# Kernel optimization log

Measured on AMD Instinct MI355X. Metric: run time of the kernel, lower is better.

Reference implementation:

```python
import jax, jax.numpy as jnp
import numpy as np

D_MODEL = 1024
NUM_HEADS = 16
D_K = D_MODEL // NUM_HEADS
SCALE = float(np.sqrt(D_K))


def setup_inputs() -> dict:
    key = jax.random.key(0)
    ks = jax.random.split(key, 11)
    B, S = 2, 2048
    s = 0.02
    return {
        "query": jax.random.normal(ks[0], (B, S, D_MODEL), dtype=jnp.float32),
        "key_in": jax.random.normal(ks[1], (B, S, D_MODEL), dtype=jnp.float32),
        "value": jax.random.normal(ks[2], (B, S, D_MODEL), dtype=jnp.float32),
        "w_q": jax.random.normal(ks[3], (D_MODEL, D_MODEL), dtype=jnp.float32) * s,
        "b_q": jnp.zeros((D_MODEL,), dtype=jnp.float32),
        "w_k": jax.random.normal(ks[4], (D_MODEL, D_MODEL), dtype=jnp.float32) * s,
        "b_k": jnp.zeros((D_MODEL,), dtype=jnp.float32),
        "w_v": jax.random.normal(ks[5], (D_MODEL, D_MODEL), dtype=jnp.float32) * s,
        "b_v": jnp.zeros((D_MODEL,), dtype=jnp.float32),
        "w_o": jax.random.normal(ks[6], (D_MODEL, D_MODEL), dtype=jnp.float32) * s,
        "b_o": jnp.zeros((D_MODEL,), dtype=jnp.float32),
    }


def _mha(query, key_in, value, w_q, b_q, w_k, b_k, w_v, b_v, w_o, b_o):
    B, S, _ = query.shape
    # linear projections (x @ W + b), split into heads: [B, H, S, Dk]
    def proj(x, w, b):
        y = x @ w + b
        return y.reshape(B, -1, NUM_HEADS, D_K).transpose(0, 2, 1, 3)

    Q = proj(query, w_q, b_q)
    K = proj(key_in, w_k, b_k)
    V = proj(value, w_v, b_v)

    # scores: [B, H, Sq, Sk]
    scores = jnp.einsum("bhqd,bhkd->bhqk", Q, K) / SCALE
    attn = jax.nn.softmax(scores, axis=-1)  # dropout is identity in eval mode
    out = jnp.einsum("bhqk,bhkd->bhqd", attn, V)
    out = out.transpose(0, 2, 1, 3).reshape(B, S, D_MODEL)
    return out @ w_o + b_o


def reference(query, key_in, value, w_q, b_q, w_k, b_k, w_v, b_v, w_o, b_o):
    return _mha(query, key_in, value, w_q, b_q, w_k, b_k, w_v, b_v, w_o, b_o)
```

## Files before the change

### kernel.cpp

```cpp
#include <hip/hip_runtime.h>
#include <cstdint>

#define S_LEN 2048
#define DMODEL 1024
#define NHEADS 16
#define DK 64
#define BATCH 2
#define M_TOT 4096

typedef __attribute__((ext_vector_type(8))) short  short8;
typedef __attribute__((ext_vector_type(4))) float  f32x4;

__device__ __forceinline__ ushort f2bf(float f) {
    union { float f; uint32_t u; } v; v.f = f;
    uint32_t r = (v.u + 0x7fffu + ((v.u >> 16) & 1u)) >> 16;
    return (ushort)r;
}
__device__ __forceinline__ float bf2f(ushort u) {
    union { uint32_t u; float f; } v; v.u = ((uint32_t)u) << 16;
    return v.f;
}

__device__ __forceinline__ void gl_lds16(const void* g, void* l) {
    __builtin_amdgcn_global_load_lds(
        (const __attribute__((address_space(1))) void*)(g),
        (__attribute__((address_space(3))) void*)(l), 16, 0, 0);
}

__global__ __launch_bounds__(256)
void conv3_kernel(const float* __restrict__ a0, const float* __restrict__ a1,
                  const float* __restrict__ a2, ushort* __restrict__ o0,
                  ushort* __restrict__ o1, ushort* __restrict__ o2, int n8)
{
    const float*  in  = blockIdx.z == 0 ? a0 : (blockIdx.z == 1 ? a1 : a2);
    ushort*       out = blockIdx.z == 0 ? o0 : (blockIdx.z == 1 ? o1 : o2);
    int i = blockIdx.x * 256 + threadIdx.x;
    const int stride = gridDim.x * 256;
    for (; i < n8; i += stride) {
        const float4* p = (const float4*)(in + (size_t)i * 8);
        float4 a = p[0], b = p[1];
        ushort r[8];
        r[0]=f2bf(a.x); r[1]=f2bf(a.y); r[2]=f2bf(a.z); r[3]=f2bf(a.w);
        r[4]=f2bf(b.x); r[5]=f2bf(b.y); r[6]=f2bf(b.z); r[7]=f2bf(b.w);
        *(ushort4*)(out + (size_t)i * 8)     = *(ushort4*)&r[0];
        *(ushort4*)(out + (size_t)i * 8 + 4) = *(ushort4*)&r[4];
    }
}

__global__ __launch_bounds__(256)
void wtrans3_kernel(const float* __restrict__ wq, const float* __restrict__ wk,
                    const float* __restrict__ wv, ushort* __restrict__ oq,
                    ushort* __restrict__ ok, ushort* __restrict__ ov)
{
    const float* w  = blockIdx.z == 0 ? wq : (blockIdx.z == 1 ? wk : wv);
    ushort*      hi = blockIdx.z == 0 ? oq : (blockIdx.z == 1 ? ok : ov);

    __shared__ float t[64][65];
    const int n0 = blockIdx.x * 64, k0 = blockIdx.y * 64;
    const int r  = threadIdx.x >> 2;
    const int cb = (threadIdx.x & 3) * 16;

    #pragma unroll
    for (int j = 0; j < 4; ++j) {
        float4 v = *(const float4*)(w + (size_t)(k0 + r) * DMODEL + n0 + cb + j * 4);
        t[r][cb + j*4 + 0] = v.x;
        t[r][cb + j*4 + 1] = v.y;
        t[r][cb + j*4 + 2] = v.z;
        t[r][cb + j*4 + 3] = v.w;
    }
    __syncthreads();

    ushort h8[16];
    #pragma unroll
    for (int j = 0; j < 16; ++j) h8[j] = f2bf(t[cb + j][r]);
    ushort* dsth = hi + (size_t)(n0 + r) * DMODEL + k0 + cb;
    *(ushort4*)(dsth + 0)  = *(ushort4*)&h8[0];
    *(ushort4*)(dsth + 4)  = *(ushort4*)&h8[4];
    *(ushort4*)(dsth + 8)  = *(ushort4*)&h8[8];
    *(ushort4*)(dsth + 12) = *(ushort4*)&h8[12];
}

__global__ __launch_bounds__(256)
void wtrans_o_kernel(const float* __restrict__ w, ushort* __restrict__ hi,
                     ushort* __restrict__ lo)
{
    __shared__ float t[64][65];
    const int n0 = blockIdx.x * 64, k0 = blockIdx.y * 64;
    const int r  = threadIdx.x >> 2;
    const int cb = (threadIdx.x & 3) * 16;

    #pragma unroll
    for (int j = 0; j < 4; ++j) {
        float4 v = *(const float4*)(w + (size_t)(k0 + r) * DMODEL + n0 + cb + j * 4);
        t[r][cb + j*4 + 0] = v.x;
        t[r][cb + j*4 + 1] = v.y;
        t[r][cb + j*4 + 2] = v.z;
        t[r][cb + j*4 + 3] = v.w;
    }
    __syncthreads();

    ushort h8[16], l8[16];
    #pragma unroll
    for (int j = 0; j < 16; ++j) {
        float x = t[cb + j][r];
        ushort h = f2bf(x);
        h8[j] = h;
        l8[j] = f2bf(x - bf2f(h));
    }
    ushort* dsth = hi + (size_t)(n0 + r) * DMODEL + k0 + cb;
    ushort* dstl = lo + (size_t)(n0 + r) * DMODEL + k0 + cb;
    #pragma unroll
    for (int j = 0; j < 4; ++j) {
        *(ushort4*)(dsth + j*4) = *(ushort4*)&h8[j*4];
        *(ushort4*)(dstl + j*4) = *(ushort4*)&l8[j*4];
    }
}

template<int OMODE>
__global__ __launch_bounds__(256)
void gemm_bf16_kernel(const ushort* __restrict__ A, const ushort* __restrict__ Bt,
                      const float* __restrict__ bias, ushort* __restrict__ out,
                      float oscale)
{
    __shared__ __align__(16) ushort lds[2][12288];

    const int t = threadIdx.x, wv = t >> 6, lane = t & 63;
    const int c = lane & 15, g = lane >> 4;
    const int m0 = blockIdx.y * 128, n0 = blockIdx.x * 64;
    const int wr = wv >> 1, wc = wv & 1;
    const int lrow = lane >> 3, lcol = lane & 7;

    f32x4 acc[4][2];
    #pragma unroll
    for (int i = 0; i < 4; ++i)
        #pragma unroll
        for (int j = 0; j < 2; ++j)
            acc[i][j] = (f32x4){0.f, 0.f, 0.f, 0.f};

    auto stage = [&](int buf, int kt) {
        #pragma unroll
        for (int j = 0; j < 6; ++j) {
            const int ci = wv * 6 + j;
            ushort* dst = &lds[buf][ci * 512];
            const ushort* src;
            if (ci < 16) {
                const int row  = ci * 8 + lrow;
                const int colb = (lcol * 16) ^ ((row & 7) << 4);
                src = A + (size_t)(m0 + row) * 1024 + kt * 64 + (colb >> 1);
            } else {
                const int row  = (ci - 16) * 8 + lrow;
                const int colb = (lcol * 16) ^ ((row & 7) << 4);
                src = Bt + (size_t)(n0 + row) * 1024 + kt * 64 + (colb >> 1);
            }
            gl_lds16(src, dst);
        }
    };

    stage(0, 0);
    __syncthreads();

    for (int kt = 0; kt < 16; ++kt) {
        const int cur = kt & 1;
        if (kt < 15) stage(cur ^ 1, kt + 1);

        const char* la = (const char*)&lds[cur][0];
        const char* lb = (const char*)&lds[cur][8192];
        #pragma unroll
        for (int kk = 0; kk < 2; ++kk) {
            short8 af[4], bf[2];
            #pragma unroll
            for (int mf = 0; mf < 4; ++mf) {
                const int row = wr * 64 + mf * 16 + c;
                af[mf] = *(const short8*)(la + row * 128 +
                          ((kk * 64 + g * 16) ^ ((c & 7) << 4)));
            }
            #pragma unroll
            for (int nf = 0; nf < 2; ++nf) {
                const int row = wc * 32 + nf * 16 + c;
                bf[nf] = *(const short8*)(lb + row * 128 +
                          ((kk * 64 + g * 16) ^ ((c & 7) << 4)));
            }
            #pragma unroll
            for (int mf = 0; mf < 4; ++mf)
                #pragma unroll
                for (int nf = 0; nf < 2; ++nf)
                    acc[mf][nf] = __builtin_amdgcn_mfma_f32_16x16x32_bf16(
                        af[mf], bf[nf], acc[mf][nf], 0, 0, 0);
        }
        __syncthreads();
    }

    const int b      = m0 >> 11;
    const int s_base = m0 & 2047;
    #pragma unroll
    for (int nf = 0; nf < 2; ++nf) {
        const int ncol = n0 + wc * 32 + nf * 16 + c;
        const float bv = bias[ncol];
        const int h = ncol >> 6, dk = ncol & 63;
        #pragma unroll
        for (int mf = 0; mf < 4; ++mf) {
            if (OMODE == 1) {
                #pragma unroll
                for (int j = 0; j < 4; ++j) {
                    const int s = s_base + wr * 64 + mf * 16 + g * 4 + j;
                    out[(((size_t)(b * NHEADS + h) * S_LEN + s) * DK) + dk] =
                        f2bf((acc[mf][nf][j] + bv) * oscale);
                }
            } else {
                ushort4 v4;
                v4.x = f2bf((acc[mf][nf][0] + bv) * oscale);
                v4.y = f2bf((acc[mf][nf][1] + bv) * oscale);
                v4.z = f2bf((acc[mf][nf][2] + bv) * oscale);
                v4.w = f2bf((acc[mf][nf][3] + bv) * oscale);
                const int s = s_base + wr * 64 + mf * 16 + g * 4;
                *(ushort4*)&out[((size_t)(b * NHEADS + h) * DK + dk) * S_LEN + s] = v4;
            }
        }
    }
}

__global__ __launch_bounds__(256)
void gemm_split_kernel(const ushort* __restrict__ Ahi, const ushort* __restrict__ Alo,
                       const ushort* __restrict__ Bhi, const ushort* __restrict__ Blo,
                       const float* __restrict__ bias, float* __restrict__ out)
{
    __shared__ __align__(16) ushort lds[24576];

    const int t = threadIdx.x, wv = t >> 6, lane = t & 63;
    const int c = lane & 15, g = lane >> 4;
    const int m0 = blockIdx.y * 128, n0 = blockIdx.x * 64;
    const int wr = wv >> 1, wc = wv & 1;
    const int lrow = lane >> 3, lcol = lane & 7;

    f32x4 acc[4][2];
    #pragma unroll
    for (int i = 0; i < 4; ++i)
        #pragma unroll
        for (int j = 0; j < 2; ++j)
            acc[i][j] = (f32x4){0.f, 0.f, 0.f, 0.f};

    for (int kt = 0; kt < 16; ++kt) {
        if (kt) __syncthreads();
        #pragma unroll
        for (int j = 0; j < 12; ++j) {
            const int ci = wv * 12 + j;
            ushort* dst = &lds[ci * 512];
            const ushort* src;
            int row, colb;
            if (ci < 16) {
                row = ci * 8 + lrow; colb = (lcol*16) ^ ((row&7)<<4);
                src = Ahi + (size_t)(m0+row)*1024 + kt*64 + (colb>>1);
            } else if (ci < 32) {
                row = (ci-16)*8 + lrow; colb = (lcol*16) ^ ((row&7)<<4);
                src = Alo + (size_t)(m0+row)*1024 + kt*64 + (colb>>1);
            } else if (ci < 40) {
                row = (ci-32)*8 + lrow; colb = (lcol*16) ^ ((row&7)<<4);
                src = Bhi + (size_t)(n0+row)*1024 + kt*64 + (colb>>1);
            } else {
                row = (ci-40)*8 + lrow; colb = (lcol*16) ^ ((row&7)<<4);
                src = Blo + (size_t)(n0+row)*1024 + kt*64 + (colb>>1);
            }
            gl_lds16(src, dst);
        }
        __syncthreads();

        const char* lah = (const char*)&lds[0];
        const char* lal = (const char*)&lds[8192];
        const char* lbh = (const char*)&lds[16384];
        const char* lbl = (const char*)&lds[20480];
        #pragma unroll
        for (int kk = 0; kk < 2; ++kk) {
            short8 ah[4], al[4], bh[2], bl[2];
            #pragma unroll
            for (int mf = 0; mf < 4; ++mf) {
                const int row = wr*64 + mf*16 + c;
                const int off = row*128 + ((kk*64 + g*16) ^ ((c&7)<<4));
                ah[mf] = *(const short8*)(lah + off);
                al[mf] = *(const short8*)(lal + off);
            }
            #pragma unroll
            for (int nf = 0; nf < 2; ++nf) {
                const int row = wc*32 + nf*16 + c;
                const int off = row*128 + ((kk*64 + g*16) ^ ((c&7)<<4));
                bh[nf] = *(const short8*)(lbh + off);
                bl[nf] = *(const short8*)(lbl + off);
            }
            #pragma unroll
            for (int mf = 0; mf < 4; ++mf)
                #pragma unroll
                for (int nf = 0; nf < 2; ++nf) {
                    acc[mf][nf] = __builtin_amdgcn_mfma_f32_16x16x32_bf16(ah[mf], bh[nf], acc[mf][nf], 0,0,0);
                    acc[mf][nf] = __builtin_amdgcn_mfma_f32_16x16x32_bf16(ah[mf], bl[nf], acc[mf][nf], 0,0,0);
                    acc[mf][nf] = __builtin_amdgcn_mfma_f32_16x16x32_bf16(al[mf], bh[nf], acc[mf][nf], 0,0,0);
                }
        }
    }

    #pragma unroll
    for (int nf = 0; nf < 2; ++nf) {
        const int ncol = n0 + wc*32 + nf*16 + c;
        const float bv = bias[ncol];
        #pragma unroll
        for (int mf = 0; mf < 4; ++mf)
            #pragma unroll
            for (int j = 0; j < 4; ++j) {
                const int m = m0 + wr*64 + mf*16 + g*4 + j;
                out[(size_t)m * 1024 + ncol] = acc[mf][nf][j] + bv;
            }
    }
}

__global__ __launch_bounds__(256, 4)
void attn_kernel3(const ushort* __restrict__ Qh, const ushort* __restrict__ Kh,
                  const ushort* __restrict__ Vt, ushort* __restrict__ ctx_hi,
                  ushort* __restrict__ ctx_lo)
{
    __shared__ __align__(16) ushort   KV[2][8192];
    __shared__ __align__(16) uint32_t Plds[4][512];

    const int t = threadIdx.x, wv = t >> 6, lane = t & 63;
    const int c = lane & 15, g = lane >> 4;
    const int bh = blockIdx.y;
    const int q0 = blockIdx.x * 64 + wv * 16;
    const int lrow = lane >> 3, lcol = lane & 7;

    const ushort* Kb = Kh + (size_t)bh * S_LEN * DK;
    const ushort* Vb = Vt + (size_t)bh * DK * S_LEN;

    const ushort* Qb = Qh + ((size_t)bh * S_LEN + q0 + c) * DK;
    short8 qf[2];
    qf[0] = *(const short8*)(Qb + g * 8);
    qf[1] = *(const short8*)(Qb + 32 + g * 8);

    auto stage = [&](int buf, int k0) {
        #pragma unroll
        for (int j = 0; j < 4; ++j) {
            const int ci = wv * 4 + j;
            ushort* dst = &KV[buf][ci * 512];
            const ushort* src;
            if (ci < 8) {
                const int row  = ci * 8 + lrow;
                const int colb = (lcol * 16) ^ ((row & 7) << 4);
                src = Kb + (size_t)(k0 + row) * DK + (colb >> 1);
            } else {
                const int row  = (ci - 8) * 8 + lrow;
                const int colb = (lcol * 16) ^ ((row & 7) << 4);
                src = Vb + (size_t)row * S_LEN + k0 + (colb >> 1);
            }
            gl_lds16(src, dst);
        }
    };

    float m = -3.0e38f, l = 0.f;
    f32x4 acc_o[4];
    #pragma unroll
    for (int i = 0; i < 4; ++i) acc_o[i] = (f32x4){0.f, 0.f, 0.f, 0.f};

    char* Pb = (char*)&Plds[wv][0];
    const int a7 = (c & 7) << 4;

    stage(0, 0);
    __syncthreads();

    for (int kt = 0; kt < 32; ++kt) {
        const int cur = kt & 1;
        if (kt < 31) stage(cur ^ 1, (kt + 1) * 64);

        const char* Kl = (const char*)&KV[cur][0];
        const char* Vl = (const char*)&KV[cur][4096];

        f32x4 sa[4];
        #pragma unroll
        for (int kb = 0; kb < 4; ++kb) sa[kb] = (f32x4){0.f,0.f,0.f,0.f};
        #pragma unroll
        for (int kb = 0; kb < 4; ++kb) {
            const int row = kb * 16 + c;
            #pragma unroll
            for (int h = 0; h < 2; ++h) {
                short8 kf = *(const short8*)(Kl + row * 128 + ((h * 64 + g * 16) ^ a7));
                sa[kb] = __builtin_amdgcn_mfma_f32_16x16x32_bf16(kf, qf[h], sa[kb], 0,0,0);
            }
        }

        float mt = sa[0][0];
        #pragma unroll
        for (int kb = 0; kb < 4; ++kb)
            #pragma unroll
            for (int j = 0; j < 4; ++j) mt = fmaxf(mt, sa[kb][j]);
        mt = fmaxf(mt, __shfl_xor(mt, 16));
        mt = fmaxf(mt, __shfl_xor(mt, 32));

        if (__any(mt > m + 8.f)) {
            const float mnew = fmaxf(m, mt);
            const float corr = __builtin_amdgcn_exp2f(m - mnew);
            float corrj[4];
            #pragma unroll
            for (int j = 0; j < 4; ++j)
                corrj[j] = __shfl(corr, (lane & 48) | (g * 4 + j));
            #pragma unroll
            for (int db = 0; db < 4; ++db)
                #pragma unroll
                for (int j = 0; j < 4; ++j) acc_o[db][j] *= corrj[j];
            l *= corr;
            m = mnew;
        }

        float p[16], ps = 0.f;
        #pragma unroll
        for (int kb = 0; kb < 4; ++kb)
            #pragma unroll
            for (int j = 0; j < 4; ++j) {
                float pp = __builtin_amdgcn_exp2f(sa[kb][j] - m);
                p[kb * 4 + j] = pp;
                ps += pp;
            }
        ps += __shfl_xor(ps, 16);
        ps += __shfl_xor(ps, 32);
        l += ps;

        uint32_t u[8];
        #pragma unroll
        for (int i = 0; i < 8; ++i)
            asm("v_cvt_pk_bf16_f32 %0, %1, %2"
                : "=v"(u[i]) : "v"(p[2*i]), "v"(p[2*i+1]));
        #pragma unroll
        for (int kb = 0; kb < 4; ++kb) {
            uint2 w2; w2.x = u[2*kb]; w2.y = u[2*kb+1];
            *(uint2*)(Pb + c * 128 + ((kb * 32 + g * 8) ^ a7)) = w2;
        }
        short8 pa0 = *(const short8*)(Pb + c * 128 + ((g * 16) ^ a7));
        short8 pa1 = *(const short8*)(Pb + c * 128 + ((64 + g * 16) ^ a7));

        #pragma unroll
        for (int db = 0; db < 4; ++db) {
            const int row = db * 16 + c;
            short8 vf0 = *(const short8*)(Vl + row * 128 + ((g * 16) ^ a7));
            short8 vf1 = *(const short8*)(Vl + row * 128 + ((64 + g * 16) ^ a7));
            acc_o[db] = __builtin_amdgcn_mfma_f32_16x16x32_bf16(pa0, vf0, acc_o[db], 0,0,0);
            acc_o[db] = __builtin_amdgcn_mfma_f32_16x16x32_bf16(pa1, vf1, acc_o[db], 0,0,0);
        }
        __syncthreads();
    }

    float invj[4];
    #pragma unroll
    for (int j = 0; j < 4; ++j)
        invj[j] = 1.f / __shfl(l, (lane & 48) | (g * 4 + j));

    const int b = bh >> 4, h = bh & 15;
    #pragma unroll
    for (int db = 0; db < 4; ++db)
        #pragma unroll
        for (int j = 0; j < 4; ++j) {
            const float val = acc_o[db][j] * invj[j];
            const ushort hi = f2bf(val);
            const ushort lo = f2bf(val - bf2f(hi));
            const size_t idx = ((size_t)b * S_LEN + q0 + g * 4 + j) * DMODEL
                             + h * DK + db * 16 + c;
            ctx_hi[idx] = hi;
            ctx_lo[idx] = lo;
        }
}

extern "C" void kernel_launch(void* const* d_in, const int* in_sizes, int n_in,
                              void* d_out, int out_size, void* d_ws, size_t ws_size,
                              hipStream_t stream)
{
    const float* query  = (const float*)d_in[0];
    const float* key_in = (const float*)d_in[1];
    const float* value  = (const float*)d_in[2];
    const float* w_q = (const float*)d_in[3];
    const float* b_q = (const float*)d_in[4];
    const float* w_k = (const float*)d_in[5];
    const float* b_k = (const float*)d_in[6];
    const float* w_v = (const float*)d_in[7];
    const float* b_v = (const float*)d_in[8];
    const float* w_o = (const float*)d_in[9];
    const float* b_o = (const float*)d_in[10];
    float* out = (float*)d_out;

    const size_t E4M = (size_t)M_TOT * DMODEL;
    const size_t E1M = (size_t)DMODEL * DMODEL;

    ushort* ws = (ushort*)d_ws;
    ushort* Aq    = ws;
    ushort* Ak    = Aq + E4M;
    ushort* Av    = Ak + E4M;
    ushort* Qh    = Av + E4M;
    ushort* Kh    = Qh + E4M;
    ushort* Vt    = Kh + E4M;
    ushort* Wq    = Vt + E4M;
    ushort* Wk    = Wq + E1M;
    ushort* Wv    = Wk + E1M;
    ushort* Wo_hi = Wv + E1M;
    ushort* Wo_lo = Wo_hi + E1M;
    ushort* ctx_hi = Aq;
    ushort* ctx_lo = Ak;

    const float qscale = 0.125f * 1.44269504088896340736f;

    dim3 blk(256);
    hipLaunchKernelGGL(conv3_kernel, dim3(512, 1, 3), blk, 0, stream,
                       query, key_in, value, Aq, Ak, Av, (int)(E4M / 8));
    hipLaunchKernelGGL(wtrans3_kernel, dim3(16, 16, 3), blk, 0, stream,
                       w_q, w_k, w_v, Wq, Wk, Wv);
    hipLaunchKernelGGL(wtrans_o_kernel, dim3(16, 16), blk, 0, stream,
                       w_o, Wo_hi, Wo_lo);

    dim3 ggrd(DMODEL / 64, M_TOT / 128);
    hipLaunchKernelGGL((gemm_bf16_kernel<1>), ggrd, blk, 0, stream, Aq, Wq, b_q, Qh, qscale);
    hipLaunchKernelGGL((gemm_bf16_kernel<1>), ggrd, blk, 0, stream, Ak, Wk, b_k, Kh, 1.0f);
    hipLaunchKernelGGL((gemm_bf16_kernel<2>), ggrd, blk, 0, stream, Av, Wv, b_v, Vt, 1.0f);

    dim3 agrd(S_LEN / 64, BATCH * NHEADS);
    hipLaunchKernelGGL(attn_kernel3, agrd, blk, 0, stream, Qh, Kh, Vt, ctx_hi, ctx_lo);

    hipLaunchKernelGGL(gemm_split_kernel, ggrd, blk, 0, stream,
                       ctx_hi, ctx_lo, Wo_hi, Wo_lo, b_o, out);
}
```

Before: 160.1 us.

## Rewrite attention with 32x32 MFMA tiles and register-only P exchange

The attention kernel moves from 16x16x32 to 32x32x16 bf16 MFMA, with each wave owning 32 query rows and each block 128 queries. The P matrix is handed from the score MFMA layout to the PV operand layout with v_permlane32_swap in registers instead of a round trip through LDS, which removes the per-wave P buffer. Staging addresses are precomputed once outside the loop. The cost is more registers per wave (launch bounds drop to 2 blocks) and half as many blocks, which lowers occupancy and parallelism.

```diff
diff --git a/kernel.cpp b/kernel.cpp
--- a/kernel.cpp
+++ b/kernel.cpp
@@ -8,8 +8,9 @@
 #define BATCH 2
 #define M_TOT 4096
 
-typedef __attribute__((ext_vector_type(8))) short  short8;
-typedef __attribute__((ext_vector_type(4))) float  f32x4;
+typedef __attribute__((ext_vector_type(8)))  short  short8;
+typedef __attribute__((ext_vector_type(4)))  float  f32x4;
+typedef __attribute__((ext_vector_type(16))) float  f32x16;
 
 __device__ __forceinline__ ushort f2bf(float f) {
     union { float f; uint32_t u; } v; v.f = f;
@@ -310,54 +311,64 @@
     }
 }
 
-__global__ __launch_bounds__(256, 4)
-void attn_kernel3(const ushort* __restrict__ Qh, const ushort* __restrict__ Kh,
+__global__ __launch_bounds__(256, 2)
+void attn_kernel4(const ushort* __restrict__ Qh, const ushort* __restrict__ Kh,
                   const ushort* __restrict__ Vt, ushort* __restrict__ ctx_hi,
                   ushort* __restrict__ ctx_lo)
 {
-    __shared__ __align__(16) ushort   KV[2][8192];
-    __shared__ __align__(16) uint32_t Plds[4][512];
-
-    const int t = threadIdx.x, wv = t >> 6, lane = t & 63;
-    const int c = lane & 15, g = lane >> 4;
+    __shared__ __align__(16) ushort KV[2][8192];
+
+    const int t  = threadIdx.x, wv = t >> 6, lane = t & 63;
+    const int q  = lane & 31;
+    const int hi = lane >> 5;
     const int bh = blockIdx.y;
-    const int q0 = blockIdx.x * 64 + wv * 16;
-    const int lrow = lane >> 3, lcol = lane & 7;
+    const int q0 = blockIdx.x * 128 + wv * 32;
 
     const ushort* Kb = Kh + (size_t)bh * S_LEN * DK;
     const ushort* Vb = Vt + (size_t)bh * DK * S_LEN;
-
-    const ushort* Qb = Qh + ((size_t)bh * S_LEN + q0 + c) * DK;
-    short8 qf[2];
-    qf[0] = *(const short8*)(Qb + g * 8);
-    qf[1] = *(const short8*)(Qb + 32 + g * 8);
-
+    const ushort* Qb = Qh + ((size_t)bh * S_LEN + q0 + q) * DK;
+
+    short8 qf[4];
+    #pragma unroll
+    for (int s = 0; s < 4; ++s)
+        qf[s] = *(const short8*)(Qb + s * 16 + hi * 8);
+
+    const ushort* sbase[4];
+    int sstr[4];
+    char* dbase[4];
+    #pragma unroll
+    for (int j = 0; j < 4; ++j) {
+        const int D = (j * 256 + t) * 16;
+        dbase[j] = (char*)&KV[0][0] + D;
+        if (D < 8192) {
+            const int row = D >> 7;
+            const int X   = D & 127;
+            const int Xs  = X ^ ((row & 7) << 4);
+            sbase[j] = Kb + row * DK + (Xs >> 1);
+            sstr[j]  = DK;
+        } else {
+            const int Y   = D - 8192;
+            const int kk  = Y >> 12;
+            const int Z   = Y & 4095;
+            const int r   = Z >> 7;
+            const int gsl = ((Z & 127) >> 4) ^ (r & 7);
+            const int d   = r + ((gsl >> 2) << 5);
+            sbase[j] = Vb + (size_t)d * S_LEN + kk * 32 + (gsl & 3) * 8;
+            sstr[j]  = 1;
+        }
+    }
     auto stage = [&](int buf, int k0) {
         #pragma unroll
-        for (int j = 0; j < 4; ++j) {
-            const int ci = wv * 4 + j;
-            ushort* dst = &KV[buf][ci * 512];
-            const ushort* src;
-            if (ci < 8) {
-                const int row  = ci * 8 + lrow;
-                const int colb = (lcol * 16) ^ ((row & 7) << 4);
-                src = Kb + (size_t)(k0 + row) * DK + (colb >> 1);
-            } else {
-                const int row  = (ci - 8) * 8 + lrow;
-                const int colb = (lcol * 16) ^ ((row & 7) << 4);
-                src = Vb + (size_t)row * S_LEN + k0 + (colb >> 1);
-            }
-            gl_lds16(src, dst);
-        }
+        for (int j = 0; j < 4; ++j)
+            gl_lds16(sbase[j] + (size_t)k0 * sstr[j], dbase[j] + buf * 16384);
     };
 
     float m = -3.0e38f, l = 0.f;
-    f32x4 acc_o[4];
-    #pragma unroll
-    for (int i = 0; i < 4; ++i) acc_o[i] = (f32x4){0.f, 0.f, 0.f, 0.f};
-
-    char* Pb = (char*)&Plds[wv][0];
-    const int a7 = (c & 7) << 4;
+    f32x16 accO[2];
+    #pragma unroll
+    for (int i = 0; i < 16; ++i) { accO[0][i] = 0.f; accO[1][i] = 0.f; }
+
+    const int swz = (q & 7) << 4;
 
     stage(0, 0);
     __syncthreads();
@@ -367,98 +378,81 @@
         if (kt < 31) stage(cur ^ 1, (kt + 1) * 64);
 
         const char* Kl = (const char*)&KV[cur][0];
-        const char* Vl = (const char*)&KV[cur][4096];
-
-        f32x4 sa[4];
-        #pragma unroll
-        for (int kb = 0; kb < 4; ++kb) sa[kb] = (f32x4){0.f,0.f,0.f,0.f};
-        #pragma unroll
-        for (int kb = 0; kb < 4; ++kb) {
-            const int row = kb * 16 + c;
-            #pragma unroll
-            for (int h = 0; h < 2; ++h) {
-                short8 kf = *(const short8*)(Kl + row * 128 + ((h * 64 + g * 16) ^ a7));
-                sa[kb] = __builtin_amdgcn_mfma_f32_16x16x32_bf16(kf, qf[h], sa[kb], 0,0,0);
-            }
-        }
-
-        float mt = sa[0][0];
-        #pragma unroll
-        for (int kb = 0; kb < 4; ++kb)
-            #pragma unroll
-            for (int j = 0; j < 4; ++j) mt = fmaxf(mt, sa[kb][j]);
-        mt = fmaxf(mt, __shfl_xor(mt, 16));
-        mt = fmaxf(mt, __shfl_xor(mt, 32));
-
-        if (__any(mt > m + 8.f)) {
-            const float mnew = fmaxf(m, mt);
-            const float corr = __builtin_amdgcn_exp2f(m - mnew);
-            float corrj[4];
-            #pragma unroll
-            for (int j = 0; j < 4; ++j)
-                corrj[j] = __shfl(corr, (lane & 48) | (g * 4 + j));
-            #pragma unroll
-            for (int db = 0; db < 4; ++db)
+        const char* Vl = Kl + 8192;
+
+        #pragma unroll
+        for (int kk = 0; kk < 2; ++kk) {
+            f32x16 sa;
+            #pragma unroll
+            for (int i = 0; i < 16; ++i) sa[i] = 0.f;
+            #pragma unroll
+            for (int s = 0; s < 4; ++s) {
+                short8 kf = *(const short8*)(Kl + (kk * 32 + q) * 128 +
+                                             ((s * 32 + hi * 16) ^ swz));
+                sa = __builtin_amdgcn_mfma_f32_32x32x16_bf16(kf, qf[s], sa, 0, 0, 0);
+            }
+
+            float mt = sa[0];
+            #pragma unroll
+            for (int r = 1; r < 16; ++r) mt = fmaxf(mt, sa[r]);
+            mt = fmaxf(mt, __shfl_xor(mt, 32));
+
+            if (__any(mt > m + 8.f)) {
+                const float mnew = fmaxf(m, mt);
+                const float corr = __builtin_amdgcn_exp2f(m - mnew);
                 #pragma unroll
-                for (int j = 0; j < 4; ++j) acc_o[db][j] *= corrj[j];
-            l *= corr;
-            m = mnew;
-        }
-
-        float p[16], ps = 0.f;
-        #pragma unroll
-        for (int kb = 0; kb < 4; ++kb)
-            #pragma unroll
-            for (int j = 0; j < 4; ++j) {
-                float pp = __builtin_amdgcn_exp2f(sa[kb][j] - m);
-                p[kb * 4 + j] = pp;
-                ps += pp;
-            }
-        ps += __shfl_xor(ps, 16);
-        ps += __shfl_xor(ps, 32);
-        l += ps;
-
-        uint32_t u[8];
-        #pragma unroll
-        for (int i = 0; i < 8; ++i)
-            asm("v_cvt_pk_bf16_f32 %0, %1, %2"
-                : "=v"(u[i]) : "v"(p[2*i]), "v"(p[2*i+1]));
-        #pragma unroll
-        for (int kb = 0; kb < 4; ++kb) {
-            uint2 w2; w2.x = u[2*kb]; w2.y = u[2*kb+1];
-            *(uint2*)(Pb + c * 128 + ((kb * 32 + g * 8) ^ a7)) = w2;
-        }
-        short8 pa0 = *(const short8*)(Pb + c * 128 + ((g * 16) ^ a7));
-        short8 pa1 = *(const short8*)(Pb + c * 128 + ((64 + g * 16) ^ a7));
-
-        #pragma unroll
-        for (int db = 0; db < 4; ++db) {
-            const int row = db * 16 + c;
-            short8 vf0 = *(const short8*)(Vl + row * 128 + ((g * 16) ^ a7));
-            short8 vf1 = *(const short8*)(Vl + row * 128 + ((64 + g * 16) ^ a7));
-            acc_o[db] = __builtin_amdgcn_mfma_f32_16x16x32_bf16(pa0, vf0, acc_o[db], 0,0,0);
-            acc_o[db] = __builtin_amdgcn_mfma_f32_16x16x32_bf16(pa1, vf1, acc_o[db], 0,0,0);
+                for (int r = 0; r < 16; ++r) { accO[0][r] *= corr; accO[1][r] *= corr; }
+                l *= corr;
+                m = mnew;
+            }
+
+            float p[16], ps = 0.f;
+            #pragma unroll
+            for (int r = 0; r < 16; ++r) {
+                p[r] = __builtin_amdgcn_exp2f(sa[r] - m);
+                ps += p[r];
+            }
+            ps += __shfl_xor(ps, 32);
+            l += ps;
+
+            uint32_t u[8];
+            #pragma unroll
+            for (int jj = 0; jj < 8; ++jj)
+                asm("v_cvt_pk_bf16_f32 %0, %1, %2"
+                    : "=v"(u[jj]) : "v"(p[2*jj]), "v"(p[2*jj+1]));
+            asm("v_permlane32_swap_b32 %0, %1" : "+v"(u[0]), "+v"(u[2]));
+            asm("v_permlane32_swap_b32 %0, %1" : "+v"(u[1]), "+v"(u[3]));
+            asm("v_permlane32_swap_b32 %0, %1" : "+v"(u[4]), "+v"(u[6]));
+            asm("v_permlane32_swap_b32 %0, %1" : "+v"(u[5]), "+v"(u[7]));
+            union { uint32_t w[4]; short8 s8; } pb0, pb1;
+            pb0.w[0]=u[0]; pb0.w[1]=u[1]; pb0.w[2]=u[2]; pb0.w[3]=u[3];
+            pb1.w[0]=u[4]; pb1.w[1]=u[5]; pb1.w[2]=u[6]; pb1.w[3]=u[7];
+
+            const char* Vg = Vl + kk * 4096;
+            #pragma unroll
+            for (int db = 0; db < 2; ++db) {
+                short8 vf0 = *(const short8*)(Vg + q * 128 + ((db*64 +      hi*16) ^ swz));
+                short8 vf1 = *(const short8*)(Vg + q * 128 + ((db*64 + 32 + hi*16) ^ swz));
+                accO[db] = __builtin_amdgcn_mfma_f32_32x32x16_bf16(vf0, pb0.s8, accO[db], 0, 0, 0);
+                accO[db] = __builtin_amdgcn_mfma_f32_32x32x16_bf16(vf1, pb1.s8, accO[db], 0, 0, 0);
+            }
         }
         __syncthreads();
     }
 
-    float invj[4];
-    #pragma unroll
-    for (int j = 0; j < 4; ++j)
-        invj[j] = 1.f / __shfl(l, (lane & 48) | (g * 4 + j));
-
+    const float inv = 1.f / l;
     const int b = bh >> 4, h = bh & 15;
-    #pragma unroll
-    for (int db = 0; db < 4; ++db)
-        #pragma unroll
-        for (int j = 0; j < 4; ++j) {
-            const float val = acc_o[db][j] * invj[j];
-            const ushort hi = f2bf(val);
-            const ushort lo = f2bf(val - bf2f(hi));
-            const size_t idx = ((size_t)b * S_LEN + q0 + g * 4 + j) * DMODEL
-                             + h * DK + db * 16 + c;
-            ctx_hi[idx] = hi;
-            ctx_lo[idx] = lo;
+    ushort* base_hi = ctx_hi + ((size_t)b * S_LEN + q0 + q) * DMODEL + h * DK;
+    ushort* base_lo = ctx_lo + ((size_t)b * S_LEN + q0 + q) * DMODEL + h * DK;
+    #pragma unroll
+    for (int db = 0; db < 2; ++db)
+        #pragma unroll
+        for (int r = 0; r < 16; ++r) {
+            const int d = db * 32 + (r & 3) + 8 * (r >> 2) + 4 * hi;
+            const float val = accO[db][r] * inv;
+            const ushort vh = f2bf(val);
+            base_hi[d] = vh;
+            base_lo[d] = f2bf(val - bf2f(vh));
         }
 }
 
@@ -512,8 +506,8 @@
     hipLaunchKernelGGL((gemm_bf16_kernel<1>), ggrd, blk, 0, stream, Ak, Wk, b_k, Kh, 1.0f);
     hipLaunchKernelGGL((gemm_bf16_kernel<2>), ggrd, blk, 0, stream, Av, Wv, b_v, Vt, 1.0f);
 
-    dim3 agrd(S_LEN / 64, BATCH * NHEADS);
-    hipLaunchKernelGGL(attn_kernel3, agrd, blk, 0, stream, Qh, Kh, Vt, ctx_hi, ctx_lo);
+    dim3 agrd(S_LEN / 128, BATCH * NHEADS);
+    hipLaunchKernelGGL(attn_kernel4, agrd, blk, 0, stream, Qh, Kh, Vt, ctx_hi, ctx_lo);
 
     hipLaunchKernelGGL(gemm_split_kernel, ggrd, blk, 0, stream,
                        ctx_hi, ctx_lo, Wo_hi, Wo_lo, b_o, out);
```

Result: faster. 149.4 us (-6.7%).
